# Kernel optimization log

Measured on AMD Instinct MI355X. Metric: run time of the kernel, lower is better.

Reference implementation:

```python
import jax, jax.numpy as jnp
import numpy as np


def setup_inputs() -> dict:
    key = jax.random.key(0)
    k1, k2 = jax.random.split(key)
    N1, N2 = 16384, 16384
    pos1 = jax.random.normal(k1, (N1, 2), dtype=jnp.float32)
    pos2 = jax.random.normal(k2, (N2, 2), dtype=jnp.float32)
    return {"pos1": pos1, "pos2": pos2}


def reference(pos1, pos2):
    # pos1: [N1, 2], pos2: [N2, 2]
    diff = pos1[:, None, :] - pos2[None, :, :]          # [N1, N2, 2]
    dist = jnp.sqrt(jnp.sum(diff * diff, axis=2))       # [N1, N2]
    nearest = jnp.min(dist, axis=1)                     # [N1]
    return jnp.mean(nearest)
```

## Files before the change

kernel.cpp:

```cpp
#include <hip/hip_runtime.h>
#include <math.h>

#define N1 16384
#define N2 16384
#define BLOCK 256
#define PTS 8
#define I_BLOCKS (N1 / (BLOCK * PTS))
#define SLICES 128

__device__ __forceinline__ unsigned int f2key(float f) {
    unsigned int b = __float_as_uint(f);
    return (b & 0x80000000u) ? ~b : (b | 0x80000000u);
}
__device__ __forceinline__ float key2f(unsigned int k) {
    unsigned int b = (k & 0x80000000u) ? (k & 0x7FFFFFFFu) : ~k;
    return __uint_as_float(b);
}

__global__ __launch_bounds__(BLOCK, 4)
void nn_partial(const float2* __restrict__ pos1,
                const float4* __restrict__ pos2,
                unsigned int* __restrict__ keys,
                unsigned int* __restrict__ ticket,
                int slice_f4) {
    const int ib = blockIdx.x;
    const int sl = blockIdx.y;
    const int t  = threadIdx.x;

    if (ib == 0 && sl == 0 && t == 0) *ticket = 0;

    const float4* __restrict__ q = pos2 + (size_t)sl * slice_f4;
    const int i0 = ib * (BLOCK * PTS) + t;

    float x[PTS], y[PTS], m[PTS];
#pragma unroll
    for (int k = 0; k < PTS; ++k) {
        float2 p = pos1[i0 + k * BLOCK];
        x[k] = -2.f * p.x;
        y[k] = -2.f * p.y;
        m[k] = 3.4e38f;
    }

#pragma unroll 4
    for (int j = 0; j < slice_f4; ++j) {
        float4 qq = q[j];
        float az = fmaf(qq.x, qq.x, qq.y * qq.y);
        float bz = fmaf(qq.z, qq.z, qq.w * qq.w);
#pragma unroll
        for (int k = 0; k < PTS; ++k) {
            float ta = fmaf(x[k], qq.x, fmaf(y[k], qq.y, az));
            float tb = fmaf(x[k], qq.z, fmaf(y[k], qq.w, bz));
            m[k] = fminf(m[k], fminf(ta, tb));
        }
    }

#pragma unroll
    for (int k = 0; k < PTS; ++k) {
        atomicMin(&keys[i0 + k * BLOCK], f2key(m[k]));
    }
}

__global__ __launch_bounds__(BLOCK)
void nn_finish(const unsigned int* __restrict__ keys,
               const float2* __restrict__ pos1,
               float* __restrict__ blocksums,
               unsigned int* __restrict__ ticket,
               float* __restrict__ out) {
    const int t = threadIdx.x;
    const int i = blockIdx.x * BLOCK + t;

    float g = key2f(keys[i]);
    float2 p = pos1[i];
    float d2 = fmaxf(fmaf(p.x, p.x, p.y * p.y) + g, 0.f);
    float sum = sqrtf(d2);

    for (int off = 32; off > 0; off >>= 1) {
        sum += __shfl_down(sum, off, 64);
    }
    __shared__ float wsum[BLOCK / 64];
    __shared__ int lastflag;
    if ((t & 63) == 0) wsum[t >> 6] = sum;
    __syncthreads();
    if (t == 0) {
        float s = 0.f;
        for (int w = 0; w < BLOCK / 64; ++w) s += wsum[w];
        blocksums[blockIdx.x] = s;
        __threadfence();
        unsigned int old = atomicAdd(ticket, 1u);
        lastflag = (old == gridDim.x - 1) ? 1 : 0;
    }
    __syncthreads();
    if (lastflag && t < 64) {
        volatile float* vb = (volatile float*)blocksums;
        float v = vb[t];
        for (int off = 32; off > 0; off >>= 1) {
            v += __shfl_down(v, off, 64);
        }
        if (t == 0) out[0] = v / (float)N1;
    }
}

extern "C" void kernel_launch(void* const* d_in, const int* in_sizes, int n_in,
                              void* d_out, int out_size, void* d_ws, size_t ws_size,
                              hipStream_t stream) {
    const float2* pos1 = (const float2*)d_in[0];
    const float4* pos2 = (const float4*)d_in[1];
    float* out = (float*)d_out;

    unsigned int* keys = (unsigned int*)d_ws;
    float* blocksums   = (float*)(keys + N1);
    unsigned int* ticket = (unsigned int*)(blocksums + 64);

    const int slice_f4 = (N2 / SLICES) / 2;

    hipMemsetAsync(keys, 0xFF, (size_t)N1 * sizeof(unsigned int), stream);

    dim3 grid1(I_BLOCKS, SLICES);
    nn_partial<<<grid1, BLOCK, 0, stream>>>(pos1, pos2, keys, ticket, slice_f4);
    nn_finish<<<N1 / BLOCK, BLOCK, 0, stream>>>(keys, pos1, blocksums, ticket, out);
}
```

Measured before the change: 81.39 us.

## Fuse partial min and final reduction into one kernel with per-column tickets

Result: slower. 160.0 us (+96.6%).

```diff
diff --git a/kernel.cpp b/kernel.cpp
--- a/kernel.cpp
+++ b/kernel.cpp
@@ -4,33 +4,25 @@
 #define N1 16384
 #define N2 16384
 #define BLOCK 256
-#define PTS 8
-#define I_BLOCKS (N1 / (BLOCK * PTS))
-#define SLICES 128
-
-__device__ __forceinline__ unsigned int f2key(float f) {
-    unsigned int b = __float_as_uint(f);
-    return (b & 0x80000000u) ? ~b : (b | 0x80000000u);
-}
-__device__ __forceinline__ float key2f(unsigned int k) {
-    unsigned int b = (k & 0x80000000u) ? (k & 0x7FFFFFFFu) : ~k;
-    return __uint_as_float(b);
-}
+#define COLS 16
+#define SLICES 64
+#define PTS 4
+#define COL_PTS (BLOCK * PTS)
+#define SLICE_F4 ((N2 / SLICES) / 2)
 
 __global__ __launch_bounds__(BLOCK, 4)
-void nn_partial(const float2* __restrict__ pos1,
-                const float4* __restrict__ pos2,
-                unsigned int* __restrict__ keys,
-                unsigned int* __restrict__ ticket,
-                int slice_f4) {
-    const int ib = blockIdx.x;
-    const int sl = blockIdx.y;
-    const int t  = threadIdx.x;
+void nn_fused(const float2* __restrict__ pos1,
+              const float4* __restrict__ pos2,
+              float* __restrict__ partials,
+              float* __restrict__ blocksums,
+              unsigned int* __restrict__ tickets,
+              float* __restrict__ out) {
+    const int col = blockIdx.x;
+    const int sl  = blockIdx.y;
+    const int t   = threadIdx.x;
 
-    if (ib == 0 && sl == 0 && t == 0) *ticket = 0;
-
-    const float4* __restrict__ q = pos2 + (size_t)sl * slice_f4;
-    const int i0 = ib * (BLOCK * PTS) + t;
+    const float4* __restrict__ q = pos2 + (size_t)sl * SLICE_F4;
+    const int i0 = col * COL_PTS + t;
 
     float x[PTS], y[PTS], m[PTS];
 #pragma unroll
@@ -42,7 +34,7 @@
     }
 
 #pragma unroll 4
-    for (int j = 0; j < slice_f4; ++j) {
+    for (int j = 0; j < SLICE_F4; ++j) {
         float4 qq = q[j];
         float az = fmaf(qq.x, qq.x, qq.y * qq.y);
         float bz = fmaf(qq.z, qq.z, qq.w * qq.w);
@@ -54,25 +46,39 @@
         }
     }
 
+    float* dst = partials + (size_t)sl * N1 + i0;
 #pragma unroll
     for (int k = 0; k < PTS; ++k) {
-        atomicMin(&keys[i0 + k * BLOCK], f2key(m[k]));
+        dst[k * BLOCK] = m[k];
     }
-}
 
-__global__ __launch_bounds__(BLOCK)
-void nn_finish(const unsigned int* __restrict__ keys,
-               const float2* __restrict__ pos1,
-               float* __restrict__ blocksums,
-               unsigned int* __restrict__ ticket,
-               float* __restrict__ out) {
-    const int t = threadIdx.x;
-    const int i = blockIdx.x * BLOCK + t;
+    __threadfence();
+    __shared__ int rank;
+    if (t == 0) rank = (int)atomicAdd(&tickets[col], 1u);
+    __syncthreads();
+    if (rank != SLICES - 1) return;
+    __threadfence();
 
-    float g = key2f(keys[i]);
-    float2 p = pos1[i];
-    float d2 = fmaxf(fmaf(p.x, p.x, p.y * p.y) + g, 0.f);
-    float sum = sqrtf(d2);
+    float g[PTS];
+#pragma unroll
+    for (int k = 0; k < PTS; ++k) g[k] = 3.4e38f;
+
+#pragma unroll 4
+    for (int s2 = 0; s2 < SLICES; ++s2) {
+        const float* src = partials + (size_t)s2 * N1 + i0;
+#pragma unroll
+        for (int k = 0; k < PTS; ++k) {
+            g[k] = fminf(g[k], src[k * BLOCK]);
+        }
+    }
+
+    float sum = 0.f;
+#pragma unroll
+    for (int k = 0; k < PTS; ++k) {
+        float2 p = pos1[i0 + k * BLOCK];
+        float d2 = fmaxf(fmaf(p.x, p.x, p.y * p.y) + g[k], 0.f);
+        sum += sqrtf(d2);
+    }
 
     for (int off = 32; off > 0; off >>= 1) {
         sum += __shfl_down(sum, off, 64);
@@ -84,15 +90,16 @@
     if (t == 0) {
         float s = 0.f;
         for (int w = 0; w < BLOCK / 64; ++w) s += wsum[w];
-        blocksums[blockIdx.x] = s;
+        blocksums[col] = s;
         __threadfence();
-        unsigned int old = atomicAdd(ticket, 1u);
-        lastflag = (old == gridDim.x - 1) ? 1 : 0;
+        unsigned int old = atomicAdd(&tickets[COLS], 1u);
+        lastflag = (old == COLS - 1) ? 1 : 0;
     }
     __syncthreads();
     if (lastflag && t < 64) {
+        __threadfence();
         volatile float* vb = (volatile float*)blocksums;
-        float v = vb[t];
+        float v = (t < COLS) ? vb[t] : 0.f;
         for (int off = 32; off > 0; off >>= 1) {
             v += __shfl_down(v, off, 64);
         }
@@ -107,15 +114,13 @@
     const float4* pos2 = (const float4*)d_in[1];
     float* out = (float*)d_out;
 
-    unsigned int* keys = (unsigned int*)d_ws;
-    float* blocksums   = (float*)(keys + N1);
-    unsigned int* ticket = (unsigned int*)(blocksums + 64);
+    float* partials       = (float*)d_ws;
+    float* blocksums      = partials + (size_t)SLICES * N1;
+    unsigned int* tickets = (unsigned int*)(blocksums + COLS);
 
-    const int slice_f4 = (N2 / SLICES) / 2;
+    hipMemsetAsync(tickets, 0, (COLS + 1) * sizeof(unsigned int), stream);
 
-    hipMemsetAsync(keys, 0xFF, (size_t)N1 * sizeof(unsigned int), stream);
-
-    dim3 grid1(I_BLOCKS, SLICES);
-    nn_partial<<<grid1, BLOCK, 0, stream>>>(pos1, pos2, keys, ticket, slice_f4);
-    nn_finish<<<N1 / BLOCK, BLOCK, 0, stream>>>(keys, pos1, blocksums, ticket, out);
+    dim3 grid(COLS, SLICES);
+    nn_fused<<<grid, BLOCK, 0, stream>>>(pos1, pos2, partials, blocksums,
+                                         tickets, out);
 }
```

## Fuse finish reduction into partial kernel via per-row-block last-arriver tickets

Applied to the files above, without the earlier changes.

Measured after the change: 84.61 us. +3.9%, slower.

```diff
diff --git a/kernel.cpp b/kernel.cpp
--- a/kernel.cpp
+++ b/kernel.cpp
@@ -7,6 +7,7 @@
 #define PTS 8
 #define I_BLOCKS (N1 / (BLOCK * PTS))
 #define SLICES 128
+#define SLICE_F4 ((N2 / SLICES) / 2)
 
 __device__ __forceinline__ unsigned int f2key(float f) {
     unsigned int b = __float_as_uint(f);
@@ -18,19 +19,18 @@
 }
 
 __global__ __launch_bounds__(BLOCK, 4)
-void nn_partial(const float2* __restrict__ pos1,
-                const float4* __restrict__ pos2,
-                unsigned int* __restrict__ keys,
-                unsigned int* __restrict__ ticket,
-                int slice_f4) {
+void nn_fused(const float2* __restrict__ pos1,
+              const float4* __restrict__ pos2,
+              unsigned int* __restrict__ keys,
+              unsigned int* __restrict__ tickets,
+              float* __restrict__ blocksums,
+              float* __restrict__ out) {
     const int ib = blockIdx.x;
     const int sl = blockIdx.y;
     const int t  = threadIdx.x;
+    const int i0 = ib * (BLOCK * PTS) + t;
 
-    if (ib == 0 && sl == 0 && t == 0) *ticket = 0;
-
-    const float4* __restrict__ q = pos2 + (size_t)sl * slice_f4;
-    const int i0 = ib * (BLOCK * PTS) + t;
+    const float4* __restrict__ q = pos2 + (size_t)sl * SLICE_F4;
 
     float x[PTS], y[PTS], m[PTS];
 #pragma unroll
@@ -42,7 +42,7 @@
     }
 
 #pragma unroll 4
-    for (int j = 0; j < slice_f4; ++j) {
+    for (int j = 0; j < SLICE_F4; ++j) {
         float4 qq = q[j];
         float az = fmaf(qq.x, qq.x, qq.y * qq.y);
         float bz = fmaf(qq.z, qq.z, qq.w * qq.w);
@@ -58,21 +58,26 @@
     for (int k = 0; k < PTS; ++k) {
         atomicMin(&keys[i0 + k * BLOCK], f2key(m[k]));
     }
-}
 
-__global__ __launch_bounds__(BLOCK)
-void nn_finish(const unsigned int* __restrict__ keys,
-               const float2* __restrict__ pos1,
-               float* __restrict__ blocksums,
-               unsigned int* __restrict__ ticket,
-               float* __restrict__ out) {
-    const int t = threadIdx.x;
-    const int i = blockIdx.x * BLOCK + t;
+    asm volatile("s_waitcnt vmcnt(0)" ::: "memory");
+    __shared__ int rank;
+    if (t == 0) rank = (int)atomicAdd(&tickets[ib], 1u);
+    __syncthreads();
+    if (rank != SLICES - 2) return;
 
-    float g = key2f(keys[i]);
-    float2 p = pos1[i];
-    float d2 = fmaxf(fmaf(p.x, p.x, p.y * p.y) + g, 0.f);
-    float sum = sqrtf(d2);
+    __builtin_amdgcn_fence(__ATOMIC_ACQUIRE, "agent");
+
+    float sum = 0.f;
+#pragma unroll
+    for (int k = 0; k < PTS; ++k) {
+        unsigned int kk = __hip_atomic_load(&keys[i0 + k * BLOCK],
+                                            __ATOMIC_RELAXED,
+                                            __HIP_MEMORY_SCOPE_AGENT);
+        float g = key2f(kk);
+        float2 p = pos1[i0 + k * BLOCK];
+        float d2 = fmaxf(fmaf(p.x, p.x, p.y * p.y) + g, 0.f);
+        sum += sqrtf(d2);
+    }
 
     for (int off = 32; off > 0; off >>= 1) {
         sum += __shfl_down(sum, off, 64);
@@ -84,16 +89,19 @@
     if (t == 0) {
         float s = 0.f;
         for (int w = 0; w < BLOCK / 64; ++w) s += wsum[w];
-        blocksums[blockIdx.x] = s;
-        __threadfence();
-        unsigned int old = atomicAdd(ticket, 1u);
-        lastflag = (old == gridDim.x - 1) ? 1 : 0;
+        __hip_atomic_store(&blocksums[ib], s, __ATOMIC_RELAXED,
+                           __HIP_MEMORY_SCOPE_AGENT);
+        asm volatile("s_waitcnt vmcnt(0)" ::: "memory");
+        unsigned int old = atomicAdd(&tickets[I_BLOCKS], 1u);
+        lastflag = (old == (unsigned)(I_BLOCKS - 2)) ? 1 : 0;
     }
     __syncthreads();
     if (lastflag && t < 64) {
-        volatile float* vb = (volatile float*)blocksums;
-        float v = vb[t];
-        for (int off = 32; off > 0; off >>= 1) {
+        float v = (t < I_BLOCKS)
+            ? __hip_atomic_load(&blocksums[t], __ATOMIC_RELAXED,
+                                __HIP_MEMORY_SCOPE_AGENT)
+            : 0.f;
+        for (int off = 4; off > 0; off >>= 1) {
             v += __shfl_down(v, off, 64);
         }
         if (t == 0) out[0] = v / (float)N1;
@@ -107,15 +115,13 @@
     const float4* pos2 = (const float4*)d_in[1];
     float* out = (float*)d_out;
 
-    unsigned int* keys = (unsigned int*)d_ws;
-    float* blocksums   = (float*)(keys + N1);
-    unsigned int* ticket = (unsigned int*)(blocksums + 64);
+    unsigned int* keys    = (unsigned int*)d_ws;
+    unsigned int* tickets = keys + N1;
+    float* blocksums      = (float*)(tickets + I_BLOCKS + 1);
 
-    const int slice_f4 = (N2 / SLICES) / 2;
+    hipMemsetAsync(keys, 0xFF, (size_t)(N1 + I_BLOCKS + 1) * sizeof(unsigned int),
+                   stream);
 
-    hipMemsetAsync(keys, 0xFF, (size_t)N1 * sizeof(unsigned int), stream);
-
-    dim3 grid1(I_BLOCKS, SLICES);
-    nn_partial<<<grid1, BLOCK, 0, stream>>>(pos1, pos2, keys, ticket, slice_f4);
-    nn_finish<<<N1 / BLOCK, BLOCK, 0, stream>>>(keys, pos1, blocksums, ticket, out);
+    dim3 grid(I_BLOCKS, SLICES);
+    nn_fused<<<grid, BLOCK, 0, stream>>>(pos1, pos2, keys, tickets, blocksums, out);
 }
```
